# Performance work log

Measured on AMD Instinct MI355X. Metric: run time of the kernel, lower is better.

Reference implementation:

```python
import jax, jax.numpy as jnp
import numpy as np

N_NODES, N_GRAPHS, N_EDGES = 40960, 1024, 163840


def setup_inputs() -> dict:
    key = jax.random.key(0)
    ks = jax.random.split(key, 40)
    w = lambda k, s: jax.random.normal(k, s, jnp.float32) * 0.05
    inp = {
        "x": jax.random.normal(ks[0], (N_NODES, 78), jnp.float32),
        "edge_index": jax.random.randint(ks[1], (2, N_EDGES), 0, N_NODES, jnp.int32),
        "batch": jnp.repeat(jnp.arange(N_GRAPHS, dtype=jnp.int32), N_NODES // N_GRAPHS),
        "target1": jax.random.normal(ks[2], (N_GRAPHS, 750, 20), jnp.float32),
        "target2": jax.random.randint(ks[3], (N_GRAPHS, 750), 0, 26, jnp.int32),
        # GCN layers
        "W1": w(ks[4], (78, 78)), "b1": jnp.zeros((78,), jnp.float32),
        "W2": w(ks[5], (78, 156)), "b2": jnp.zeros((156,), jnp.float32),
        "W3": w(ks[6], (156, 312)), "b3": jnp.zeros((312,), jnp.float32),
        "Wg1": w(ks[7], (312, 1024)), "bg1": jnp.zeros((1024,), jnp.float32),
        "Wg2": w(ks[8], (1024, 128)), "bg2": jnp.zeros((128,), jnp.float32),
        # protein branch
        "emb": w(ks[9], (26, 128)),
        "Wc2": w(ks[10], (32, 750, 8)), "bc2": jnp.zeros((32,), jnp.float32),
        "Wxt2": w(ks[11], (32 * 121, 128)), "bxt2": jnp.zeros((128,), jnp.float32),
        "Wc1": w(ks[12], (32, 750, 8)), "bc1": jnp.zeros((32,), jnp.float32),
        "Wxt1": w(ks[13], (416, 128)), "bxt1": jnp.zeros((128,), jnp.float32),
        # fusion head
        "Wf1": w(ks[14], (384, 1024)), "bf1": jnp.zeros((1024,), jnp.float32),
        "Wf2": w(ks[15], (1024, 512)), "bf2": jnp.zeros((512,), jnp.float32),
        "Wo": w(ks[16], (512, 1)), "bo": jnp.zeros((1,), jnp.float32),
    }
    return inp


def _conv1d(x, w, b):
    # x: [B, C_in, L], w: [C_out, C_in, K] -> [B, C_out, L-K+1]
    y = jax.lax.conv_general_dilated(x, w, (1,), "VALID",
                                     dimension_numbers=("NCH", "OIH", "NCH"))
    return y + b[None, :, None]


def reference(x, edge_index, batch, target1, target2,
              W1, b1, W2, b2, W3, b3, Wg1, bg1, Wg2, bg2,
              emb, Wc2, bc2, Wxt2, bxt2, Wc1, bc1, Wxt1, bxt1,
              Wf1, bf1, Wf2, bf2, Wo, bo):
    N = x.shape[0]
    loop = jnp.arange(N, dtype=edge_index.dtype)
    src = jnp.concatenate([edge_index[0], loop])  # message source j
    dst = jnp.concatenate([edge_index[1], loop])  # aggregation target i
    # symmetric GCN normalization with self-loops (degree from dst, as in PyG)
    deg = jnp.zeros((N,), x.dtype).at[dst].add(1.0)
    dinv = jax.lax.rsqrt(deg)  # deg >= 1 due to self loops
    norm = (dinv[src] * dinv[dst])[:, None]

    def gcn(h, W, b):
        m = (h @ W)[src] * norm
        return jax.ops.segment_sum(m, dst, num_segments=N) + b

    h = jax.nn.relu(gcn(x, W1, b1))
    h = jax.nn.relu(gcn(h, W2, b2))
    h = jax.nn.relu(gcn(h, W3, b3))
    # global max pool per graph
    g = jax.ops.segment_max(h, batch, num_segments=N_GRAPHS)
    g = jax.nn.relu(g @ Wg1 + bg1)
    g = g @ Wg2 + bg2  # dropout is identity at inference

    # protein branch 2: embedding -> conv1d over channels=750
    e = emb[target2]                         # [B, 750, 128]
    xt2 = _conv1d(e, Wc2, bc2)               # [B, 32, 121]
    xt2 = xt2.reshape(-1, 32 * 121) @ Wxt2 + bxt2

    # protein branch 1: raw float features
    xt1 = _conv1d(target1, Wc1, bc1)         # [B, 32, 13]
    xt1 = xt1.reshape(-1, 416) @ Wxt1 + bxt1

    xc = jnp.concatenate([g, xt1, xt2], axis=1)  # [B, 384]
    xc = jax.nn.relu(xc @ Wf1 + bf1)
    xc = jax.nn.relu(xc @ Wf2 + bf2)
    return xc @ Wo + bo
```

## Files before the change

### kernel.cpp

```cpp
#include <hip/hip_runtime.h>
#include <hip/hip_bf16.h>

#define NN 40960
#define NE 163840
#define NB 1024

typedef __attribute__((ext_vector_type(8))) short short8;
typedef __attribute__((ext_vector_type(4))) short short4v;
typedef __attribute__((ext_vector_type(4))) float floatx4;

__device__ inline unsigned short f2bf(float f) {
    union { float f; unsigned u; } v; v.f = f;
    unsigned r = v.u + 0x7fffu + ((v.u >> 16) & 1u);
    return (unsigned short)(r >> 16);
}
__device__ inline float bf2f(unsigned short s) {
    union { unsigned u; float f; } v; v.u = ((unsigned)s) << 16; return v.f;
}
__device__ inline unsigned pack2bf(float lo, float hi) {
    return (unsigned)f2bf(lo) | ((unsigned)f2bf(hi) << 16);
}

static const size_t o_dinv = 0, o_g312 = 40960, o_g1024 = 360448, o_xc = 1409024,
                    o_f1 = 1802240, o_f2 = 2850816, o_b1v = 3375104, o_b2v = 3375232,
// ... 31 lines not shown
        int t = __shfl_up(s, d);
        if (l >= d) s += t;
    }
    if (l < 40) blockOff[l] = s - orig;
}

__global__ __launch_bounds__(1024) void k_scan3(int* __restrict__ off, int* __restrict__ cur,
                                                const int* __restrict__ blockOff) {
    int i = blockIdx.x * 1024 + threadIdx.x;
    int o = off[i] + blockOff[blockIdx.x];
    off[i] = o;
    cur[i] = o;
    if (i == NN - 1) off[NN] = NE;
}

__global__ void k_fill(const int* __restrict__ ei, int* __restrict__ cur, int* __restrict__ srcOut) {
    int e = blockIdx.x * 256 + threadIdx.x;
    if (e >= NE) return;
    int s = ei[e], d = ei[NE + e];
    int pos = atomicAdd(&cur[d], 1);
    srcOut[pos] = s;
}

__global__ __launch_bounds__(256) void k_cvt_wt(const float* __restrict__ W1, const float* __restrict__ W2,
                                                const float* __restrict__ W3, const float* __restrict__ Wg1,
                                                const float* __restrict__ Wg2, const float* __restrict__ Wf1,
                                                const float* __restrict__ Wf2, unsigned short* __restrict__ dst) {
    const int cum[8]  = {0, 128, 320, 640, 1664, 1792, 2816, 3328};
    const int KP[7]   = {96, 96, 160, 320, 1024, 384, 1024};
    const int KB[7]   = {78, 78, 156, 312, 1024, 384, 1024};
    const int NNm[7]  = {78, 156, 312, 1024, 128, 1024, 512};
    const size_t OFF[7] = {0, 12288, 30720, 81920, 409600, 540672, 933888};
    int m = 0;
    int bx = blockIdx.x;
    while (m < 6 && bx >= cum[m + 1]) m++;
    int r = bx - cum[m];
    const float* src = (m == 0) ? W1 : (m == 1) ? W2 : (m == 2) ? W3 : (m == 3) ? Wg1
                     : (m == 4) ? Wg2 : (m == 5) ? Wf1 : Wf2;
    int kp = KP[m], kb = KB[m], nn = NNm[m];
    unsigned short* d = dst + OFF[m] + (size_t)r * kp;
    for (int k = threadIdx.x; k < kp; k += 256) {
        float v = (r < nn && k < kb) ? src[(size_t)k * nn + r] : 0.f;
        d[k] = f2bf(v);
    }
}

__global__ __launch_bounds__(64) void k_agg_x(const float* __restrict__ x, const float* __restrict__ dinv,
                                              const int* __restrict__ off, const int* __restrict__ srcs,
                                              unsigned* __restrict__ out) {
    int n = blockIdx.x;
    int f = threadIdx.x;
    if (f >= 48) return;
    if (f >= 39) { out[(size_t)n * 48 + f] = 0; return; }
    float di = dinv[n];
    float2 sv = *(const float2*)&x[(size_t)n * 78 + 2 * f];
    float a0 = sv.x * di * di, a1 = sv.y * di * di;
    int e0 = off[n], e1 = off[n + 1];
    int e = e0;
    for (; e + 4 <= e1; e += 4) {
        int s0 = srcs[e], s1 = srcs[e + 1], s2 = srcs[e + 2], s3 = srcs[e + 3];
        float d0 = dinv[s0] * di, d1 = dinv[s1] * di, d2 = dinv[s2] * di, d3 = dinv[s3] * di;
        float2 v0 = *(const float2*)&x[(size_t)s0 * 78 + 2 * f];
        float2 v1 = *(const float2*)&x[(size_t)s1 * 78 + 2 * f];
        float2 v2 = *(const float2*)&x[(size_t)s2 * 78 + 2 * f];
        float2 v3 = *(const float2*)&x[(size_t)s3 * 78 + 2 * f];
        a0 += v0.x * d0 + v1.x * d1 + v2.x * d2 + v3.x * d3;
        a1 += v0.y * d0 + v1.y * d1 + v2.y * d2 + v3.y * d3;
    }
    for (; e < e1; e++) {
        int s = srcs[e];
        float dd = dinv[s] * di;
        float2 v = *(const float2*)&x[(size_t)s * 78 + 2 * f];
        a0 += v.x * dd; a1 += v.y * dd;
    }
    out[(size_t)n * 48 + f] = pack2bf(a0, a1);
}

__global__ void k_agg16(const unsigned* __restrict__ h, const float* __restrict__ dinv,
                        const int* __restrict__ off, const int* __restrict__ srcs,
                        unsigned* __restrict__ out, int F2) {
    int n = blockIdx.x;
    int f = threadIdx.x;
    if (f >= F2) return;
    float di = dinv[n];
    unsigned s0v = h[(size_t)n * F2 + f];
    float a0 = bf2f((unsigned short)(s0v & 0xffff)) * di * di;
    float a1 = bf2f((unsigned short)(s0v >> 16)) * di * di;
    int e0 = off[n], e1 = off[n + 1];
    int e = e0;
    for (; e + 4 <= e1; e += 4) {
        int s0 = srcs[e], s1 = srcs[e + 1], s2 = srcs[e + 2], s3 = srcs[e + 3];
        float d0 = dinv[s0] * di, d1 = dinv[s1] * di, d2 = dinv[s2] * di, d3 = dinv[s3] * di;
        unsigned v0 = h[(size_t)s0 * F2 + f];
        unsigned v1 = h[(size_t)s1 * F2 + f];
        unsigned v2 = h[(size_t)s2 * F2 + f];
        unsigned v3 = h[(size_t)s3 * F2 + f];
        a0 += bf2f((unsigned short)(v0 & 0xffff)) * d0 + bf2f((unsigned short)(v1 & 0xffff)) * d1
            + bf2f((unsigned short)(v2 & 0xffff)) * d2 + bf2f((unsigned short)(v3 & 0xffff)) * d3;
        a1 += bf2f((unsigned short)(v0 >> 16)) * d0 + bf2f((unsigned short)(v1 >> 16)) * d1
            + bf2f((unsigned short)(v2 >> 16)) * d2 + bf2f((unsigned short)(v3 >> 16)) * d3;
    }
    for (; e < e1; e++) {
        int s = srcs[e];
        float dd = dinv[s] * di;
        unsigned v = h[(size_t)s * F2 + f];
        a0 += bf2f((unsigned short)(v & 0xffff)) * dd;
        a1 += bf2f((unsigned short)(v >> 16)) * dd;
    }
    out[(size_t)n * F2 + f] = pack2bf(a0, a1);
}

__global__ void k_segmax16(const unsigned short* __restrict__ h, unsigned short* __restrict__ g) {
    int gr = blockIdx.x, f = threadIdx.x;
    if (f >= 320) return;
    if (f >= 312) { g[(size_t)gr * 320 + f] = 0; return; }
    float m = 0.0f;
    const unsigned short* base = h + (size_t)gr * 40 * 312 + f;
    for (int i = 0; i < 40; i++) m = fmaxf(m, bf2f(base[(size_t)i * 312]));
    g[(size_t)gr * 320 + f] = f2bf(m);
}

#define LDST 72
template <bool ABF16, bool OUTBF16, bool ATOMIC, bool RELU_OUT>
__global__ __launch_bounds__(256) void gemm_bt(const void* __restrict__ Av, const unsigned short* __restrict__ Bt,
                                               const float* __restrict__ bias, void* __restrict__ Cv,
                                               int Nn, int Npad, int Kpad, int Klim,
                                               int lda, int ldb, int ldc, int ksplit) {
    __shared__ __align__(16) unsigned short As[64 * LDST];
    __shared__ __align__(16) unsigned short Bs[64 * LDST];
    const float* Af = (const float*)Av;
    const unsigned short* A16 = (const unsigned short*)Av;
    float* Cf = (float*)Cv;
    unsigned short* C16 = (unsigned short*)Cv;
    int bn0 = blockIdx.x * 64;
    int bm0 = blockIdx.y * 64;
    int k0 = blockIdx.z * ksplit;
    int kend = k0 + ksplit; if (kend > Kpad) kend = Kpad;
    int tid = threadIdx.x;
    int w = tid >> 6, l = tid & 63, q = l >> 4, r = l & 15;
    int wr = w >> 1, wc = w & 1;

    floatx4 acc[2][2];
// ... 45 lines not shown
    for (int c2 = 0; c2 < 2; c2++) {
        int col = bn0 + wc * 32 + c2 * 16 + r;
        if (col >= Npad) continue;
        bool live = col < Nn;
        float bv = (bias && live) ? bias[col] : 0.f;
#pragma unroll
        for (int i = 0; i < 2; i++) {
#pragma unroll
            for (int v = 0; v < 4; v++) {
                int row = bm0 + wr * 32 + i * 16 + q * 4 + v;
                float val = live ? (acc[i][c2][v] + bv) : 0.f;
                if (RELU_OUT) val = fmaxf(val, 0.f);
                if (OUTBF16) {
                    C16[(size_t)row * ldc + col] = live ? f2bf(val) : (unsigned short)0;
                } else if (live) {
                    if (ATOMIC) atomicAdd(&Cf[(size_t)row * ldc + col], val);
                    else Cf[(size_t)row * ldc + col] = val;
                }
            }
        }
    }
}

#define T1LD 40
#define T1S  48
#define T1K  320
__global__ __launch_bounds__(256) void gemm_t1(const float* __restrict__ A, const unsigned short* __restrict__ Bt,
                                               float* __restrict__ P) {
    __shared__ __align__(16) unsigned short As[2][64 * T1LD];
    __shared__ __align__(16) unsigned short Bs[2][128 * T1LD];
    const int Klim = 15000;
    int bm0 = blockIdx.y * 64;
    int k0 = blockIdx.x * T1K;
    int tid = threadIdx.x;
    int w = tid >> 6, l = tid & 63, q = l >> 4, r = l & 15;
    int wr = w >> 1, wc = w & 1;

    floatx4 acc[2][4];
#pragma unroll
    for (int i = 0; i < 2; i++)
#pragma unroll
        for (int c = 0; c < 4; c++) acc[i][c] = (floatx4)0.0f;

    int ra = tid >> 3, ca = (tid & 7) * 4;
    int rb = tid >> 2, cb = (tid & 3) * 8;
    const float* Ap0 = A + (size_t)(bm0 + ra) * Klim + ca;
    const float* Ap1 = A + (size_t)(bm0 + ra + 32) * Klim + ca;
    const unsigned short* Bp0 = Bt + (size_t)rb * 15360 + cb;
    const unsigned short* Bp1 = Bt + (size_t)(rb + 64) * 15360 + cb;

    float4 aA0, aA1, aB0, aB1;
    short8 bA0, bA1, bB0, bB1;

    auto loadT = [&](int kt, float4& x0, float4& x1, short8& y0, short8& y1) {
        int c = kt + ca;
        if (c < Klim) {
            x0 = *(const float4*)(Ap0 + kt);
            x1 = *(const float4*)(Ap1 + kt);
        } else {
            x0 = make_float4(0.f, 0.f, 0.f, 0.f);
            x1 = make_float4(0.f, 0.f, 0.f, 0.f);
        }
        y0 = *(const short8*)(Bp0 + kt);
        y1 = *(const short8*)(Bp1 + kt);
    };
    auto stageW = [&](int buf, const float4& x0, const float4& x1, const short8& y0, const short8& y1) {
        short4v s0, s1;
        s0[0] = (short)f2bf(x0.x); s0[1] = (short)f2bf(x0.y); s0[2] = (short)f2bf(x0.z); s0[3] = (short)f2bf(x0.w);
        s1[0] = (short)f2bf(x1.x); s1[1] = (short)f2bf(x1.y); s1[2] = (short)f2bf(x1.z); s1[3] = (short)f2bf(x1.w);
        *(short4v*)&As[buf][ra * T1LD + ca] = s0;
        *(short4v*)&As[buf][(ra + 32) * T1LD + ca] = s1;
        *(short8*)&Bs[buf][rb * T1LD + cb] = y0;
        *(short8*)&Bs[buf][(rb + 64) * T1LD + cb] = y1;
    };
    auto compute = [&](int buf) {
        short8 a0 = *(const short8*)&As[buf][(wr * 32 + r) * T1LD + q * 8];
        short8 a1 = *(const short8*)&As[buf][(wr * 32 + 16 + r) * T1LD + q * 8];
        short8 b0 = *(const short8*)&Bs[buf][(wc * 64 + r) * T1LD + q * 8];
        short8 b1 = *(const short8*)&Bs[buf][(wc * 64 + 16 + r) * T1LD + q * 8];
        short8 b2 = *(const short8*)&Bs[buf][(wc * 64 + 32 + r) * T1LD + q * 8];
        short8 b3 = *(const short8*)&Bs[buf][(wc * 64 + 48 + r) * T1LD + q * 8];
        acc[0][0] = __builtin_amdgcn_mfma_f32_16x16x32_bf16(a0, b0, acc[0][0], 0, 0, 0);
        acc[0][1] = __builtin_amdgcn_mfma_f32_16x16x32_bf16(a0, b1, acc[0][1], 0, 0, 0);
        acc[0][2] = __builtin_amdgcn_mfma_f32_16x16x32_bf16(a0, b2, acc[0][2], 0, 0, 0);
        acc[0][3] = __builtin_amdgcn_mfma_f32_16x16x32_bf16(a0, b3, acc[0][3], 0, 0, 0);
        acc[1][0] = __builtin_amdgcn_mfma_f32_16x16x32_bf16(a1, b0, acc[1][0], 0, 0, 0);
        acc[1][1] = __builtin_amdgcn_mfma_f32_16x16x32_bf16(a1, b1, acc[1][1], 0, 0, 0);
        acc[1][2] = __builtin_amdgcn_mfma_f32_16x16x32_bf16(a1, b2, acc[1][2], 0, 0, 0);
        acc[1][3] = __builtin_amdgcn_mfma_f32_16x16x32_bf16(a1, b3, acc[1][3], 0, 0, 0);
    };

    loadT(k0, aA0, aA1, bA0, bA1);
    loadT(k0 + 32, aB0, aB1, bB0, bB1);
#pragma unroll
    for (int it = 0; it < T1K / 32; it += 2) {
        stageW(0, aA0, aA1, bA0, bA1);
        if (it + 2 < T1K / 32) loadT(k0 + (it + 2) * 32, aA0, aA1, bA0, bA1);
        asm volatile("s_waitcnt lgkmcnt(0)" ::: "memory");
        __builtin_amdgcn_s_barrier();
        asm volatile("" ::: "memory");
        compute(0);
        stageW(1, aB0, aB1, bB0, bB1);
        if (it + 3 < T1K / 32) loadT(k0 + (it + 3) * 32, aB0, aB1, bB0, bB1);
        asm volatile("s_waitcnt lgkmcnt(0)" ::: "memory");
        __builtin_amdgcn_s_barrier();
        asm volatile("" ::: "memory");
        compute(1);
    }

    float* Pp = P + (size_t)blockIdx.x * (1024 * 128) + (size_t)bm0 * 128;
#pragma unroll
    for (int c = 0; c < 4; c++) {
        int col = wc * 64 + c * 16 + r;
#pragma unroll
        for (int i = 0; i < 2; i++) {
#pragma unroll
            for (int v = 0; v < 4; v++) {
                int row = wr * 32 + i * 16 + q * 4 + v;
                Pp[(size_t)row * 128 + col] = acc[i][c][v];
            }
        }
    }
}

__global__ __launch_bounds__(128) void k_red_t1(const float* __restrict__ P, float* __restrict__ xc) {
    int row = blockIdx.x, j = threadIdx.x;
    const float* p = P + (size_t)row * 128 + j;
    float s = 0.f;
#pragma unroll
    for (int ks = 0; ks < T1S; ks++) s += p[(size_t)ks * (1024 * 128)];
    xc[(size_t)row * 384 + 128 + j] += s;
}

template <int OM>
__global__ __launch_bounds__(256) void gemm_mfma_batch(const float* __restrict__ A, const float* __restrict__ B,
                                                       void* __restrict__ Cv,
                                                       int M, int Nn, int K, int ldc,
                                                       long sB, long sC) {
    __shared__ __align__(16) unsigned short As[64 * LDST];
    __shared__ __align__(16) unsigned short Bs[64 * LDST];
    const float* Bm = B + (size_t)blockIdx.z * sB;
    unsigned short* C16 = (unsigned short*)Cv + (size_t)blockIdx.z * sC;
    int bn0 = blockIdx.x * 64;
    int bm0 = blockIdx.y * 64;
    int tid = threadIdx.x;
    int w = tid >> 6, l = tid & 63, q = l >> 4, r = l & 15;
    int wr = w >> 1, wc = w & 1;

    floatx4 acc[2][2];
#pragma unroll
    for (int i = 0; i < 2; i++)
#pragma unroll
        for (int c = 0; c < 2; c++) acc[i][c] = (floatx4)0.0f;

    int mA = tid >> 2, kcA = (tid & 3) * 8;
    int nB = tid >> 2, kcB = (tid & 3) * 8;
    int gmA = bm0 + mA;
    int gnB = bn0 + nB;

    for (int kt = 0; kt < K; kt += 32) {
        {
            float av[8];
            const float* Ap = A + (size_t)gmA * K + kt + kcA;
            if (gmA < M) {
#pragma unroll
// ... 22 lines not shown
        }
        __syncthreads();
        short8 a0 = *(const short8*)&As[(wr * 32 + r) * LDST + q * 8];
        short8 a1 = *(const short8*)&As[(wr * 32 + 16 + r) * LDST + q * 8];
        short8 b0 = *(const short8*)&Bs[(wc * 32 + r) * LDST + q * 8];
        short8 b1 = *(const short8*)&Bs[(wc * 32 + 16 + r) * LDST + q * 8];
        acc[0][0] = __builtin_amdgcn_mfma_f32_16x16x32_bf16(a0, b0, acc[0][0], 0, 0, 0);
        acc[0][1] = __builtin_amdgcn_mfma_f32_16x16x32_bf16(a0, b1, acc[0][1], 0, 0, 0);
        acc[1][0] = __builtin_amdgcn_mfma_f32_16x16x32_bf16(a1, b0, acc[1][0], 0, 0, 0);
        acc[1][1] = __builtin_amdgcn_mfma_f32_16x16x32_bf16(a1, b1, acc[1][1], 0, 0, 0);
        __syncthreads();
    }

#pragma unroll
    for (int c = 0; c < 2; c++) {
        int col = bn0 + wc * 32 + c * 16 + r;
        if (col >= Nn) continue;
#pragma unroll
        for (int i = 0; i < 2; i++) {
#pragma unroll
            for (int v = 0; v < 4; v++) {
                int row = bm0 + wr * 32 + i * 16 + q * 4 + v;
                if (row >= M) continue;
                if (OM == 1) C16[(size_t)row * ldc + col] = f2bf(acc[i][c][v]);
                else C16[(size_t)col * ldc + row * 20 + blockIdx.z] = f2bf(acc[i][c][v]);
            }
        }
    }
}

__global__ __launch_bounds__(256) void k_wcr_both(const float* __restrict__ Wc2, const float* __restrict__ Wc1,
                                                  float* __restrict__ Wc2r, float* __restrict__ Wc1r) {
    int cc = blockIdx.x, j = threadIdx.x;
    const float* W = (cc < 750) ? Wc2 : Wc1;
    float* Wr = (cc < 750) ? Wc2r : Wc1r;
    int c = (cc < 750) ? cc : cc - 750;
    Wr[(size_t)c * 256 + j] = W[(size_t)(j >> 3) * 6000 + c * 8 + (j & 7)];
}

__global__ __launch_bounds__(128) void k_T_build(const float* __restrict__ emb, const float* __restrict__ Wxt2,
                                                 float* __restrict__ T) {
    __shared__ float el[128];
    int v = blockIdx.x >> 5, o = blockIdx.x & 31, j = threadIdx.x;
    el[j] = emb[(size_t)v * 128 + j];
    __syncthreads();
    float acc[8] = {};
    for (int l = 0; l < 121; l++) {
        float w = Wxt2[(size_t)(o * 121 + l) * 128 + j];
#pragma unroll
        for (int k = 0; k < 8; k++) acc[k] += el[l + k] * w;
    }
#pragma unroll
    for (int k = 0; k < 8; k++) T[(size_t)(v * 256 + o * 8 + k) * 128 + j] = acc[k];
}

__global__ __launch_bounds__(128) void k_bt_build(const float* __restrict__ Wxt1, float* __restrict__ Bt) {
    int ok = blockIdx.x, t = blockIdx.y, j = threadIdx.x;
    int o = ok >> 3, k = ok & 7, lpos = t - k;
    float v = (lpos >= 0 && lpos < 13) ? Wxt1[(size_t)(o * 13 + lpos) * 128 + j] : 0.f;
    Bt[(size_t)(t * 256 + ok) * 128 + j] = v;
}

__global__ __launch_bounds__(128) void k_u_gather16(const int* __restrict__ t2, const unsigned short* __restrict__ U,
                                                    const float* __restrict__ b2v, float* __restrict__ xc) {
    __shared__ int offs[752];
    __shared__ float red[8][128];
    int b = blockIdx.x, tid = threadIdx.x;
    int rg = tid >> 4, lane = tid & 15;
    const int* t2b = t2 + (size_t)b * 750;
    for (int i = tid; i < 750; i += 128) offs[i] = i * 3328 + t2b[i] * 128;
    __syncthreads();
    float a[8] = {};
#pragma unroll 4
    for (int i = rg; i < 750; i += 8) {
        short8 v = *(const short8*)&U[(size_t)offs[i] + lane * 8];
#pragma unroll
        for (int c = 0; c < 8; c++) a[c] += bf2f((unsigned short)v[c]);
    }
#pragma unroll
    for (int c = 0; c < 8; c++) red[rg][lane * 8 + c] = a[c];
    __syncthreads();
    float s = b2v[tid];
#pragma unroll
    for (int g = 0; g < 8; g++) s += red[g][tid];
    xc[(size_t)b * 384 + 256 + tid] = s;
}

__global__ void k_bias_init(const float* __restrict__ bxt1, const float* __restrict__ bxt2,
                            float* __restrict__ b1v, float* __restrict__ b2v) {
    int j = threadIdx.x;
    b1v[j] = bxt1[j];
    b2v[j] = bxt2[j];
}

__global__ __launch_bounds__(128) void k_bias_acc_both(const float* __restrict__ bc1, const float* __restrict__ Wxt1,
                                                       float* __restrict__ b1v,
                                                       const float* __restrict__ bc2, const float* __restrict__ Wxt2,
                                                       float* __restrict__ b2v) {
    int b = blockIdx.x, j = threadIdx.x;
    if (b < 32) {
        const float* p = Wxt1 + (size_t)b * 13 * 128 + j;
        float t = 0.f;
        for (int l = 0; l < 13; l++) t += p[(size_t)l * 128];
        atomicAdd(&b1v[j], bc1[b] * t);
    } else {
        int o = b - 32;
        const float* p = Wxt2 + (size_t)o * 121 * 128 + j;
        float t = 0.f;
        for (int l = 0; l < 121; l++) t += p[(size_t)l * 128];
        atomicAdd(&b2v[j], bc2[o] * t);
    }
}

__global__ __launch_bounds__(768) void k_initC(float* __restrict__ xc, float* __restrict__ f2,
                                               const float* __restrict__ bg2, const float* __restrict__ b1v,
                                               const float* __restrict__ bf2) {
    int b = blockIdx.x, t = threadIdx.x;
    if (t < 128) xc[(size_t)b * 384 + t] = bg2[t];
    else if (t < 256) xc[(size_t)b * 384 + t] = b1v[t - 128];
    else f2[(size_t)b * 512 + t - 256] = bf2[t - 256];
}

__global__ __launch_bounds__(64) void k_final(const float* __restrict__ f2, const float* __restrict__ Wo,
                                              const float* __restrict__ bo, float* __restrict__ out) {
    int b = blockIdx.x, lane = threadIdx.x;
    float s = 0.f;
    for (int j = lane; j < 512; j += 64) s += fmaxf(f2[(size_t)b * 512 + j], 0.f) * Wo[j];
    for (int off = 32; off; off >>= 1) s += __shfl_down(s, off);
    if (lane == 0) out[b] = s + bo[0];
}

extern "C" void kernel_launch(void* const* d_in, const int* in_sizes, int n_in,
                              void* d_out, int out_size, void* d_ws, size_t ws_size,
// ... 32 lines not shown
    float* ws = (float*)d_ws;
    float* dinv  = ws + o_dinv;
    unsigned short* g312b = (unsigned short*)(ws + o_g312);
    unsigned short* g1024b = (unsigned short*)(ws + o_g1024);
    float* xc    = ws + o_xc;
    unsigned short* f1b = (unsigned short*)(ws + o_f1);
    float* f2    = ws + o_f2;
    float* b1v   = ws + o_b1v;
    float* b2v   = ws + o_b2v;
    int* csrOff  = (int*)(ws + o_iws);
    int* csrCur  = csrOff + (NN + 1);
    int* csrSrc  = csrCur + NN;
    int* blockSum = (int*)(ws + o_f1 + 600000);
    int* blockOff = blockSum + 40;
    float* bufA  = ws + o_bufA;
    float* bufB  = ws + o_bufB;
    float* T    = bufA;
    unsigned short* U16  = (unsigned short*)(bufA + 851968);
    unsigned short* Vt16 = (unsigned short*)(bufA + 2200000);
    unsigned short* Wt   = (unsigned short*)(bufA + 3200000);
    float* Wc2r = bufA + 4000000;
    float* Wc1r = bufA + 4200000;
    float* Btb  = bufA + 4400000;
    unsigned* aggb = (unsigned*)bufB;
    unsigned short* h16 = (unsigned short*)(bufB + 5500000);
    float* Pt1 = bufB;

    unsigned short* W1t  = Wt + 0;
    unsigned short* W2t  = Wt + 12288;
    unsigned short* W3t  = Wt + 30720;
    unsigned short* Wg1t = Wt + 81920;
    unsigned short* Wg2t = Wt + 409600;
    unsigned short* Wf1t = Wt + 540672;
    unsigned short* Wf2t = Wt + 933888;

    hipMemsetAsync(csrCur, 0, NN * sizeof(int), stream);
    k_hist<<<NE / 256, 256, 0, stream>>>(ei + NE, csrCur);
    k_scan1<<<40, 1024, 0, stream>>>(csrCur, csrOff, blockSum, dinv);
    k_scan2<<<1, 64, 0, stream>>>(blockSum, blockOff);
    k_scan3<<<40, 1024, 0, stream>>>(csrOff, csrCur, blockOff);
    k_fill<<<NE / 256, 256, 0, stream>>>(ei, csrCur, csrSrc);
    k_cvt_wt<<<3328, 256, 0, stream>>>(W1, W2, W3, Wg1, Wg2, Wf1, Wf2, Wt);

    k_agg_x<<<NN, 64, 0, stream>>>(x, dinv, csrOff, csrSrc, aggb);
    gemm_bt<true, true, false, true><<<dim3(2, 640, 1), 256, 0, stream>>>(
        aggb, W1t, b1, h16, 78, 96, 96, 96, 96, 96, 96, 96);
    k_agg16<<<NN, 64, 0, stream>>>((unsigned*)h16, dinv, csrOff, csrSrc, aggb, 48);
    gemm_bt<true, true, false, true><<<dim3(3, 640, 1), 256, 0, stream>>>(
        aggb, W2t, b2, h16, 156, 160, 96, 96, 96, 96, 160, 96);
    k_agg16<<<NN, 128, 0, stream>>>((unsigned*)h16, dinv, csrOff, csrSrc, aggb, 80);
    gemm_bt<true, true, false, true><<<dim3(5, 640, 1), 256, 0, stream>>>(
        aggb, W3t, b3, h16, 312, 312, 160, 160, 160, 160, 312, 160);
    k_segmax16<<<NB, 320, 0, stream>>>(h16, g312b);
    gemm_bt<true, true, false, true><<<dim3(16, 16, 1), 256, 0, stream>>>(
        g312b, Wg1t, bg1, g1024b, 1024, 1024, 320, 320, 320, 320, 1024, 320);

    k_bias_init<<<1, 128, 0, stream>>>(bxt1, bxt2, b1v, b2v);
    k_bias_acc_both<<<64, 128, 0, stream>>>(bc1, Wxt1, b1v, bc2, Wxt2, b2v);
    k_initC<<<NB, 768, 0, stream>>>(xc, f2, bg2, b1v, bf2);

    gemm_bt<true, false, true, false><<<dim3(2, 16, 8), 256, 0, stream>>>(
        g1024b, Wg2t, nullptr, xc + 0, 128, 128, 1024, 1024, 1024, 1024, 384, 128);

    k_wcr_both<<<1500, 256, 0, stream>>>(Wc2, Wc1, Wc2r, Wc1r);
    k_T_build<<<26 * 32, 128, 0, stream>>>(emb, Wxt2, T);
    gemm_mfma_batch<1><<<dim3(2, 12, 26), 256, 0, stream>>>(Wc2r, T, U16, 750, 128, 256, 3328, 32768, 128);
    k_u_gather16<<<NB, 128, 0, stream>>>(t2, U16, b2v, xc);

    k_bt_build<<<dim3(256, 20), 128, 0, stream>>>(Wxt1, Btb);
    hipMemsetAsync(Vt16, 0, (size_t)128 * 15360 * 2, stream);
    gemm_mfma_batch<2><<<dim3(2, 12, 20), 256, 0, stream>>>(Wc1r, Btb, Vt16, 750, 128, 256, 15360, 32768, 0);
    gemm_t1<<<dim3(T1S, 16, 1), 256, 0, stream>>>(t1, Vt16, Pt1);
    k_red_t1<<<NB, 128, 0, stream>>>(Pt1, xc);

    gemm_bt<false, true, false, true><<<dim3(16, 16, 1), 256, 0, stream>>>(
        xc, Wf1t, bf1, f1b, 1024, 1024, 384, 384, 384, 384, 1024, 384);
    gemm_bt<true, false, true, false><<<dim3(8, 16, 4), 256, 0, stream>>>(
        f1b, Wf2t, nullptr, f2, 512, 512, 1024, 1024, 1024, 1024, 512, 256);
    k_final<<<NB, 64, 0, stream>>>(f2, Wo, bo, out);
}
```

Before: 458.8 us.

## Merge independent kernels into combined launches to cut launch count and overlap branches

```diff
diff --git a/kernel.cpp b/kernel.cpp
--- a/kernel.cpp
+++ b/kernel.cpp
@@ -77,65 +77,91 @@
     srcOut[pos] = s;
 }
 
-__global__ __launch_bounds__(256) void k_cvt_wt(const float* __restrict__ W1, const float* __restrict__ W2,
-                                                const float* __restrict__ W3, const float* __restrict__ Wg1,
-                                                const float* __restrict__ Wg2, const float* __restrict__ Wf1,
-                                                const float* __restrict__ Wf2, unsigned short* __restrict__ dst) {
-    const int cum[8]  = {0, 128, 320, 640, 1664, 1792, 2816, 3328};
-    const int KP[7]   = {96, 96, 160, 320, 1024, 384, 1024};
-    const int KB[7]   = {78, 78, 156, 312, 1024, 384, 1024};
-    const int NNm[7]  = {78, 156, 312, 1024, 128, 1024, 512};
-    const size_t OFF[7] = {0, 12288, 30720, 81920, 409600, 540672, 933888};
-    int m = 0;
-    int bx = blockIdx.x;
-    while (m < 6 && bx >= cum[m + 1]) m++;
-    int r = bx - cum[m];
-    const float* src = (m == 0) ? W1 : (m == 1) ? W2 : (m == 2) ? W3 : (m == 3) ? Wg1
-                     : (m == 4) ? Wg2 : (m == 5) ? Wf1 : Wf2;
-    int kp = KP[m], kb = KB[m], nn = NNm[m];
-    unsigned short* d = dst + OFF[m] + (size_t)r * kp;
-    for (int k = threadIdx.x; k < kp; k += 256) {
-        float v = (r < nn && k < kb) ? src[(size_t)k * nn + r] : 0.f;
-        d[k] = f2bf(v);
-    }
-}
-
-__global__ __launch_bounds__(64) void k_agg_x(const float* __restrict__ x, const float* __restrict__ dinv,
-                                              const int* __restrict__ off, const int* __restrict__ srcs,
-                                              unsigned* __restrict__ out) {
-    int n = blockIdx.x;
-    int f = threadIdx.x;
-    if (f >= 48) return;
-    if (f >= 39) { out[(size_t)n * 48 + f] = 0; return; }
-    float di = dinv[n];
-    float2 sv = *(const float2*)&x[(size_t)n * 78 + 2 * f];
-    float a0 = sv.x * di * di, a1 = sv.y * di * di;
-    int e0 = off[n], e1 = off[n + 1];
-    int e = e0;
-    for (; e + 4 <= e1; e += 4) {
-        int s0 = srcs[e], s1 = srcs[e + 1], s2 = srcs[e + 2], s3 = srcs[e + 3];
-        float d0 = dinv[s0] * di, d1 = dinv[s1] * di, d2 = dinv[s2] * di, d3 = dinv[s3] * di;
-        float2 v0 = *(const float2*)&x[(size_t)s0 * 78 + 2 * f];
-        float2 v1 = *(const float2*)&x[(size_t)s1 * 78 + 2 * f];
-        float2 v2 = *(const float2*)&x[(size_t)s2 * 78 + 2 * f];
-        float2 v3 = *(const float2*)&x[(size_t)s3 * 78 + 2 * f];
-        a0 += v0.x * d0 + v1.x * d1 + v2.x * d2 + v3.x * d3;
-        a1 += v0.y * d0 + v1.y * d1 + v2.y * d2 + v3.y * d3;
-    }
-    for (; e < e1; e++) {
-        int s = srcs[e];
-        float dd = dinv[s] * di;
-        float2 v = *(const float2*)&x[(size_t)s * 78 + 2 * f];
-        a0 += v.x * dd; a1 += v.y * dd;
-    }
-    out[(size_t)n * 48 + f] = pack2bf(a0, a1);
-}
-
-__global__ void k_agg16(const unsigned* __restrict__ h, const float* __restrict__ dinv,
-                        const int* __restrict__ off, const int* __restrict__ srcs,
-                        unsigned* __restrict__ out, int F2) {
-    int n = blockIdx.x;
-    int f = threadIdx.x;
+__global__ __launch_bounds__(256) void k_prep_mega(
+    const float* __restrict__ W1, const float* __restrict__ W2, const float* __restrict__ W3,
+    const float* __restrict__ Wg1, const float* __restrict__ Wg2, const float* __restrict__ Wf1,
+    const float* __restrict__ Wf2, unsigned short* __restrict__ Wt,
+    const float* __restrict__ Wc2, const float* __restrict__ Wc1,
+    float* __restrict__ Wc2r, float* __restrict__ Wc1r,
+    const float* __restrict__ Wxt1, float* __restrict__ Btb,
+    const float* __restrict__ bc1, const float* __restrict__ bxt1, float* __restrict__ b1v,
+    const float* __restrict__ bc2, const float* __restrict__ Wxt2, const float* __restrict__ bxt2,
+    float* __restrict__ b2v,
+    const float* __restrict__ emb, float* __restrict__ T) {
+    __shared__ float el[128];
+    __shared__ float bsum[2][128];
+    int bx = blockIdx.x, tid = threadIdx.x;
+    if (bx < 3328) {
+        const int cum[8]  = {0, 128, 320, 640, 1664, 1792, 2816, 3328};
+        const int KP[7]   = {96, 96, 160, 320, 1024, 384, 1024};
+        const int KB[7]   = {78, 78, 156, 312, 1024, 384, 1024};
+        const int NNm[7]  = {78, 156, 312, 1024, 128, 1024, 512};
+        const size_t OFF[7] = {0, 12288, 30720, 81920, 409600, 540672, 933888};
+        int m = 0;
+        while (m < 6 && bx >= cum[m + 1]) m++;
+        int r = bx - cum[m];
+        const float* src = (m == 0) ? W1 : (m == 1) ? W2 : (m == 2) ? W3 : (m == 3) ? Wg1
+                         : (m == 4) ? Wg2 : (m == 5) ? Wf1 : Wf2;
+        int kp = KP[m], kb = KB[m], nn = NNm[m];
+        unsigned short* d = Wt + OFF[m] + (size_t)r * kp;
+        for (int k = tid; k < kp; k += 256) {
+            float v = (r < nn && k < kb) ? src[(size_t)k * nn + r] : 0.f;
+            d[k] = f2bf(v);
+        }
+    } else if (bx < 4828) {
+        int cc = bx - 3328, j = tid;
+        const float* W = (cc < 750) ? Wc2 : Wc1;
+        float* Wr = (cc < 750) ? Wc2r : Wc1r;
+        int c = (cc < 750) ? cc : cc - 750;
+        Wr[(size_t)c * 256 + j] = W[(size_t)(j >> 3) * 6000 + c * 8 + (j & 7)];
+    } else if (bx < 7388) {
+        int idx = (bx - 4828) * 256 + tid;
+        int j = idx & 127, ok = (idx >> 7) & 255, t = idx >> 15;
+        int o = ok >> 3, k = ok & 7, lpos = t - k;
+        float v = (lpos >= 0 && lpos < 13) ? Wxt1[(size_t)(o * 13 + lpos) * 128 + j] : 0.f;
+        Btb[(size_t)(t * 256 + ok) * 128 + j] = v;
+    } else if (bx == 7388) {
+        int o2 = tid >> 7, j = tid & 127;
+        float p = 0.f;
+        for (int o = o2; o < 32; o += 2) {
+            float t = 0.f;
+            for (int l = 0; l < 13; l++) t += Wxt1[(size_t)(o * 13 + l) * 128 + j];
+            p += bc1[o] * t;
+        }
+        bsum[o2][j] = p;
+        __syncthreads();
+        if (tid < 128) b1v[j] = bxt1[j] + bsum[0][j] + bsum[1][j];
+    } else if (bx == 7389) {
+        int o2 = tid >> 7, j = tid & 127;
+        float p = 0.f;
+        for (int o = o2; o < 32; o += 2) {
+            float t = 0.f;
+            for (int l = 0; l < 121; l++) t += Wxt2[(size_t)(o * 121 + l) * 128 + j];
+            p += bc2[o] * t;
+        }
+        bsum[o2][j] = p;
+        __syncthreads();
+        if (tid < 128) b2v[j] = bxt2[j] + bsum[0][j] + bsum[1][j];
+    } else {
+        int tb = bx - 7390;
+        int v = tb >> 4, op = tb & 15;
+        int o = op * 2 + (tid >> 7), j = tid & 127;
+        if (tid < 128) el[j] = emb[(size_t)v * 128 + j];
+        __syncthreads();
+        float acc[8] = {};
+        for (int l = 0; l < 121; l++) {
+            float w = Wxt2[(size_t)(o * 121 + l) * 128 + j];
+#pragma unroll
+            for (int k = 0; k < 8; k++) acc[k] += el[l + k] * w;
+        }
+#pragma unroll
+        for (int k = 0; k < 8; k++) T[(size_t)(v * 256 + o * 8 + k) * 128 + j] = acc[k];
+    }
+}
+
+__device__ inline void d_agg16_node(int n, int f, const unsigned* __restrict__ h,
+                                    const float* __restrict__ dinv, const int* __restrict__ off,
+                                    const int* __restrict__ srcs, unsigned* __restrict__ out, int F2) {
     if (f >= F2) return;
     float di = dinv[n];
     unsigned s0v = h[(size_t)n * F2 + f];
@@ -165,14 +191,10 @@
     out[(size_t)n * F2 + f] = pack2bf(a0, a1);
 }
 
-__global__ void k_segmax16(const unsigned short* __restrict__ h, unsigned short* __restrict__ g) {
-    int gr = blockIdx.x, f = threadIdx.x;
-    if (f >= 320) return;
-    if (f >= 312) { g[(size_t)gr * 320 + f] = 0; return; }
-    float m = 0.0f;
-    const unsigned short* base = h + (size_t)gr * 40 * 312 + f;
-    for (int i = 0; i < 40; i++) m = fmaxf(m, bf2f(base[(size_t)i * 312]));
-    g[(size_t)gr * 320 + f] = f2bf(m);
+__global__ void k_agg16(const unsigned* __restrict__ h, const float* __restrict__ dinv,
+                        const int* __restrict__ off, const int* __restrict__ srcs,
+                        unsigned* __restrict__ out, int F2) {
+    d_agg16_node(blockIdx.x, threadIdx.x, h, dinv, off, srcs, out, F2);
 }
 
 #define LDST 72
@@ -264,125 +286,19 @@
     }
 }
 
-#define T1LD 40
-#define T1S  48
-#define T1K  320
-__global__ __launch_bounds__(256) void gemm_t1(const float* __restrict__ A, const unsigned short* __restrict__ Bt,
-                                               float* __restrict__ P) {
-    __shared__ __align__(16) unsigned short As[2][64 * T1LD];
-    __shared__ __align__(16) unsigned short Bs[2][128 * T1LD];
-    const int Klim = 15000;
-    int bm0 = blockIdx.y * 64;
-    int k0 = blockIdx.x * T1K;
-    int tid = threadIdx.x;
-    int w = tid >> 6, l = tid & 63, q = l >> 4, r = l & 15;
-    int wr = w >> 1, wc = w & 1;
-
-    floatx4 acc[2][4];
-#pragma unroll
-    for (int i = 0; i < 2; i++)
-#pragma unroll
-        for (int c = 0; c < 4; c++) acc[i][c] = (floatx4)0.0f;
-
-    int ra = tid >> 3, ca = (tid & 7) * 4;
-    int rb = tid >> 2, cb = (tid & 3) * 8;
-    const float* Ap0 = A + (size_t)(bm0 + ra) * Klim + ca;
-    const float* Ap1 = A + (size_t)(bm0 + ra + 32) * Klim + ca;
-    const unsigned short* Bp0 = Bt + (size_t)rb * 15360 + cb;
-    const unsigned short* Bp1 = Bt + (size_t)(rb + 64) * 15360 + cb;
-
-    float4 aA0, aA1, aB0, aB1;
-    short8 bA0, bA1, bB0, bB1;
-
-    auto loadT = [&](int kt, float4& x0, float4& x1, short8& y0, short8& y1) {
-        int c = kt + ca;
-        if (c < Klim) {
-            x0 = *(const float4*)(Ap0 + kt);
-            x1 = *(const float4*)(Ap1 + kt);
-        } else {
-            x0 = make_float4(0.f, 0.f, 0.f, 0.f);
-            x1 = make_float4(0.f, 0.f, 0.f, 0.f);
-        }
-        y0 = *(const short8*)(Bp0 + kt);
-        y1 = *(const short8*)(Bp1 + kt);
-    };
-    auto stageW = [&](int buf, const float4& x0, const float4& x1, const short8& y0, const short8& y1) {
-        short4v s0, s1;
-        s0[0] = (short)f2bf(x0.x); s0[1] = (short)f2bf(x0.y); s0[2] = (short)f2bf(x0.z); s0[3] = (short)f2bf(x0.w);
-        s1[0] = (short)f2bf(x1.x); s1[1] = (short)f2bf(x1.y); s1[2] = (short)f2bf(x1.z); s1[3] = (short)f2bf(x1.w);
-        *(short4v*)&As[buf][ra * T1LD + ca] = s0;
-        *(short4v*)&As[buf][(ra + 32) * T1LD + ca] = s1;
-        *(short8*)&Bs[buf][rb * T1LD + cb] = y0;
-        *(short8*)&Bs[buf][(rb + 64) * T1LD + cb] = y1;
-    };
-    auto compute = [&](int buf) {
-        short8 a0 = *(const short8*)&As[buf][(wr * 32 + r) * T1LD + q * 8];
-        short8 a1 = *(const short8*)&As[buf][(wr * 32 + 16 + r) * T1LD + q * 8];
-        short8 b0 = *(const short8*)&Bs[buf][(wc * 64 + r) * T1LD + q * 8];
-        short8 b1 = *(const short8*)&Bs[buf][(wc * 64 + 16 + r) * T1LD + q * 8];
-        short8 b2 = *(const short8*)&Bs[buf][(wc * 64 + 32 + r) * T1LD + q * 8];
-        short8 b3 = *(const short8*)&Bs[buf][(wc * 64 + 48 + r) * T1LD + q * 8];
-        acc[0][0] = __builtin_amdgcn_mfma_f32_16x16x32_bf16(a0, b0, acc[0][0], 0, 0, 0);
-        acc[0][1] = __builtin_amdgcn_mfma_f32_16x16x32_bf16(a0, b1, acc[0][1], 0, 0, 0);
-        acc[0][2] = __builtin_amdgcn_mfma_f32_16x16x32_bf16(a0, b2, acc[0][2], 0, 0, 0);
-        acc[0][3] = __builtin_amdgcn_mfma_f32_16x16x32_bf16(a0, b3, acc[0][3], 0, 0, 0);
-        acc[1][0] = __builtin_amdgcn_mfma_f32_16x16x32_bf16(a1, b0, acc[1][0], 0, 0, 0);
-        acc[1][1] = __builtin_amdgcn_mfma_f32_16x16x32_bf16(a1, b1, acc[1][1], 0, 0, 0);
-        acc[1][2] = __builtin_amdgcn_mfma_f32_16x16x32_bf16(a1, b2, acc[1][2], 0, 0, 0);
-        acc[1][3] = __builtin_amdgcn_mfma_f32_16x16x32_bf16(a1, b3, acc[1][3], 0, 0, 0);
-    };
-
-    loadT(k0, aA0, aA1, bA0, bA1);
-    loadT(k0 + 32, aB0, aB1, bB0, bB1);
-#pragma unroll
-    for (int it = 0; it < T1K / 32; it += 2) {
-        stageW(0, aA0, aA1, bA0, bA1);
-        if (it + 2 < T1K / 32) loadT(k0 + (it + 2) * 32, aA0, aA1, bA0, bA1);
-        asm volatile("s_waitcnt lgkmcnt(0)" ::: "memory");
-        __builtin_amdgcn_s_barrier();
-        asm volatile("" ::: "memory");
-        compute(0);
-        stageW(1, aB0, aB1, bB0, bB1);
-        if (it + 3 < T1K / 32) loadT(k0 + (it + 3) * 32, aB0, aB1, bB0, bB1);
-        asm volatile("s_waitcnt lgkmcnt(0)" ::: "memory");
-        __builtin_amdgcn_s_barrier();
-        asm volatile("" ::: "memory");
-        compute(1);
-    }
-
-    float* Pp = P + (size_t)blockIdx.x * (1024 * 128) + (size_t)bm0 * 128;
-#pragma unroll
-    for (int c = 0; c < 4; c++) {
-        int col = wc * 64 + c * 16 + r;
-#pragma unroll
-        for (int i = 0; i < 2; i++) {
-#pragma unroll
-            for (int v = 0; v < 4; v++) {
-                int row = wr * 32 + i * 16 + q * 4 + v;
-                Pp[(size_t)row * 128 + col] = acc[i][c][v];
-            }
-        }
-    }
-}
-
-__global__ __launch_bounds__(128) void k_red_t1(const float* __restrict__ P, float* __restrict__ xc) {
-    int row = blockIdx.x, j = threadIdx.x;
-    const float* p = P + (size_t)row * 128 + j;
-    float s = 0.f;
-#pragma unroll
-    for (int ks = 0; ks < T1S; ks++) s += p[(size_t)ks * (1024 * 128)];
-    xc[(size_t)row * 384 + 128 + j] += s;
-}
-
-template <int OM>
-__global__ __launch_bounds__(256) void gemm_mfma_batch(const float* __restrict__ A, const float* __restrict__ B,
-                                                       void* __restrict__ Cv,
-                                                       int M, int Nn, int K, int ldc,
-                                                       long sB, long sC) {
+__global__ __launch_bounds__(256) void k_batch_both(const float* __restrict__ Wc2r, const float* __restrict__ T,
+                                                    const float* __restrict__ Wc1r, const float* __restrict__ Btb,
+                                                    unsigned short* __restrict__ U16, unsigned short* __restrict__ Vt16) {
     __shared__ __align__(16) unsigned short As[64 * LDST];
     __shared__ __align__(16) unsigned short Bs[64 * LDST];
-    const float* Bm = B + (size_t)blockIdx.z * sB;
-    unsigned short* C16 = (unsigned short*)Cv + (size_t)blockIdx.z * sC;
+    const int M = 750, Nn = 128, K = 256;
+    int z = blockIdx.z;
+    bool om1 = z < 26;
+    const float* A = om1 ? Wc2r : Wc1r;
+    const float* Bm = om1 ? (T + (size_t)z * 32768) : (Btb + (size_t)(z - 26) * 32768);
+    unsigned short* C16 = om1 ? (U16 + (size_t)z * 128) : Vt16;
+    int ldc = om1 ? 3328 : 15360;
+    int zz = z - 26;
     int bn0 = blockIdx.x * 64;
     int bm0 = blockIdx.y * 64;
     int tid = threadIdx.x;
@@ -451,93 +367,199 @@
             for (int v = 0; v < 4; v++) {
                 int row = bm0 + wr * 32 + i * 16 + q * 4 + v;
                 if (row >= M) continue;
-                if (OM == 1) C16[(size_t)row * ldc + col] = f2bf(acc[i][c][v]);
-                else C16[(size_t)col * ldc + row * 20 + blockIdx.z] = f2bf(acc[i][c][v]);
+                if (om1) C16[(size_t)row * ldc + col] = f2bf(acc[i][c][v]);
+                else C16[(size_t)col * ldc + row * 20 + zz] = f2bf(acc[i][c][v]);
             }
         }
     }
 }
 
-__global__ __launch_bounds__(256) void k_wcr_both(const float* __restrict__ Wc2, const float* __restrict__ Wc1,
-                                                  float* __restrict__ Wc2r, float* __restrict__ Wc1r) {
-    int cc = blockIdx.x, j = threadIdx.x;
-    const float* W = (cc < 750) ? Wc2 : Wc1;
-    float* Wr = (cc < 750) ? Wc2r : Wc1r;
-    int c = (cc < 750) ? cc : cc - 750;
-    Wr[(size_t)c * 256 + j] = W[(size_t)(j >> 3) * 6000 + c * 8 + (j & 7)];
-}
-
-__global__ __launch_bounds__(128) void k_T_build(const float* __restrict__ emb, const float* __restrict__ Wxt2,
-                                                 float* __restrict__ T) {
-    __shared__ float el[128];
-    int v = blockIdx.x >> 5, o = blockIdx.x & 31, j = threadIdx.x;
-    el[j] = emb[(size_t)v * 128 + j];
-    __syncthreads();
-    float acc[8] = {};
-    for (int l = 0; l < 121; l++) {
-        float w = Wxt2[(size_t)(o * 121 + l) * 128 + j];
-#pragma unroll
-        for (int k = 0; k < 8; k++) acc[k] += el[l + k] * w;
-    }
-#pragma unroll
-    for (int k = 0; k < 8; k++) T[(size_t)(v * 256 + o * 8 + k) * 128 + j] = acc[k];
-}
-
-__global__ __launch_bounds__(128) void k_bt_build(const float* __restrict__ Wxt1, float* __restrict__ Bt) {
-    int ok = blockIdx.x, t = blockIdx.y, j = threadIdx.x;
-    int o = ok >> 3, k = ok & 7, lpos = t - k;
-    float v = (lpos >= 0 && lpos < 13) ? Wxt1[(size_t)(o * 13 + lpos) * 128 + j] : 0.f;
-    Bt[(size_t)(t * 256 + ok) * 128 + j] = v;
-}
-
-__global__ __launch_bounds__(128) void k_u_gather16(const int* __restrict__ t2, const unsigned short* __restrict__ U,
-                                                    const float* __restrict__ b2v, float* __restrict__ xc) {
+#define T1LD 40
+#define T1S  48
+#define T1K  320
+__global__ __launch_bounds__(256) void k_aggx_t1(
+    const float* __restrict__ x, const float* __restrict__ dinv, const int* __restrict__ off,
+    const int* __restrict__ srcs, unsigned* __restrict__ aggb,
+    const float* __restrict__ t1A, const unsigned short* __restrict__ Bt, float* __restrict__ P) {
+    __shared__ __align__(16) unsigned short As[2][64 * T1LD];
+    __shared__ __align__(16) unsigned short Bs[2][128 * T1LD];
+    int bx = blockIdx.x, tid = threadIdx.x;
+    if (bx < 768) {
+        const int Klim = 15000;
+        int mt = bx & 15, ks = bx >> 4;
+        int bm0 = mt * 64;
+        int k0 = ks * T1K;
+        int w = tid >> 6, l = tid & 63, q = l >> 4, r = l & 15;
+        int wr = w >> 1, wc = w & 1;
+
+        floatx4 acc[2][4];
+#pragma unroll
+        for (int i = 0; i < 2; i++)
+#pragma unroll
+            for (int c = 0; c < 4; c++) acc[i][c] = (floatx4)0.0f;
+
+        int ra = tid >> 3, ca = (tid & 7) * 4;
+        int rb = tid >> 2, cb = (tid & 3) * 8;
+        const float* Ap0 = t1A + (size_t)(bm0 + ra) * Klim + ca;
+        const float* Ap1 = t1A + (size_t)(bm0 + ra + 32) * Klim + ca;
+        const unsigned short* Bp0 = Bt + (size_t)rb * 15360 + cb;
+        const unsigned short* Bp1 = Bt + (size_t)(rb + 64) * 15360 + cb;
+
+        float4 aA0, aA1, aB0, aB1;
+        short8 bA0, bA1, bB0, bB1;
+
+        auto loadT = [&](int kt, float4& x0, float4& x1, short8& y0, short8& y1) {
+            int c = kt + ca;
+            if (c < Klim) {
+                x0 = *(const float4*)(Ap0 + kt);
+                x1 = *(const float4*)(Ap1 + kt);
+            } else {
+                x0 = make_float4(0.f, 0.f, 0.f, 0.f);
+                x1 = make_float4(0.f, 0.f, 0.f, 0.f);
+            }
+            y0 = *(const short8*)(Bp0 + kt);
+            y1 = *(const short8*)(Bp1 + kt);
+        };
+        auto stageW = [&](int buf, const float4& x0, const float4& x1, const short8& y0, const short8& y1) {
+            short4v s0, s1;
+            s0[0] = (short)f2bf(x0.x); s0[1] = (short)f2bf(x0.y); s0[2] = (short)f2bf(x0.z); s0[3] = (short)f2bf(x0.w);
+            s1[0] = (short)f2bf(x1.x); s1[1] = (short)f2bf(x1.y); s1[2] = (short)f2bf(x1.z); s1[3] = (short)f2bf(x1.w);
+            *(short4v*)&As[buf][ra * T1LD + ca] = s0;
+            *(short4v*)&As[buf][(ra + 32) * T1LD + ca] = s1;
+            *(short8*)&Bs[buf][rb * T1LD + cb] = y0;
+            *(short8*)&Bs[buf][(rb + 64) * T1LD + cb] = y1;
+        };
+        auto compute = [&](int buf) {
+            short8 a0 = *(const short8*)&As[buf][(wr * 32 + r) * T1LD + q * 8];
+            short8 a1 = *(const short8*)&As[buf][(wr * 32 + 16 + r) * T1LD + q * 8];
+            short8 b0 = *(const short8*)&Bs[buf][(wc * 64 + r) * T1LD + q * 8];
+            short8 b1 = *(const short8*)&Bs[buf][(wc * 64 + 16 + r) * T1LD + q * 8];
+            short8 b2 = *(const short8*)&Bs[buf][(wc * 64 + 32 + r) * T1LD + q * 8];
+            short8 b3 = *(const short8*)&Bs[buf][(wc * 64 + 48 + r) * T1LD + q * 8];
+            acc[0][0] = __builtin_amdgcn_mfma_f32_16x16x32_bf16(a0, b0, acc[0][0], 0, 0, 0);
+            acc[0][1] = __builtin_amdgcn_mfma_f32_16x16x32_bf16(a0, b1, acc[0][1], 0, 0, 0);
+            acc[0][2] = __builtin_amdgcn_mfma_f32_16x16x32_bf16(a0, b2, acc[0][2], 0, 0, 0);
+            acc[0][3] = __builtin_amdgcn_mfma_f32_16x16x32_bf16(a0, b3, acc[0][3], 0, 0, 0);
+            acc[1][0] = __builtin_amdgcn_mfma_f32_16x16x32_bf16(a1, b0, acc[1][0], 0, 0, 0);
+            acc[1][1] = __builtin_amdgcn_mfma_f32_16x16x32_bf16(a1, b1, acc[1][1], 0, 0, 0);
+            acc[1][2] = __builtin_amdgcn_mfma_f32_16x16x32_bf16(a1, b2, acc[1][2], 0, 0, 0);
+            acc[1][3] = __builtin_amdgcn_mfma_f32_16x16x32_bf16(a1, b3, acc[1][3], 0, 0, 0);
+        };
+
+        loadT(k0, aA0, aA1, bA0, bA1);
+        loadT(k0 + 32, aB0, aB1, bB0, bB1);
+#pragma unroll
+        for (int it = 0; it < T1K / 32; it += 2) {
+            stageW(0, aA0, aA1, bA0, bA1);
+            if (it + 2 < T1K / 32) loadT(k0 + (it + 2) * 32, aA0, aA1, bA0, bA1);
+            asm volatile("s_waitcnt lgkmcnt(0)" ::: "memory");
+            __builtin_amdgcn_s_barrier();
+            asm volatile("" ::: "memory");
+            compute(0);
+            stageW(1, aB0, aB1, bB0, bB1);
+            if (it + 3 < T1K / 32) loadT(k0 + (it + 3) * 32, aB0, aB1, bB0, bB1);
+            asm volatile("s_waitcnt lgkmcnt(0)" ::: "memory");
+            __builtin_amdgcn_s_barrier();
+            asm volatile("" ::: "memory");
+            compute(1);
+        }
+
+        float* Pp = P + (size_t)ks * (1024 * 128) + (size_t)bm0 * 128;
+#pragma unroll
+        for (int c = 0; c < 4; c++) {
+            int col = wc * 64 + c * 16 + r;
+#pragma unroll
+            for (int i = 0; i < 2; i++) {
+#pragma unroll
+                for (int v = 0; v < 4; v++) {
+                    int row = wr * 32 + i * 16 + q * 4 + v;
+                    Pp[(size_t)row * 128 + col] = acc[i][c][v];
+                }
+            }
+        }
+    } else {
+        int n = (bx - 768) * 4 + (tid >> 6);
+        int f = tid & 63;
+        if (f >= 48) return;
+        if (f >= 39) { aggb[(size_t)n * 48 + f] = 0; return; }
+        float di = dinv[n];
+        float2 sv = *(const float2*)&x[(size_t)n * 78 + 2 * f];
+        float a0 = sv.x * di * di, a1 = sv.y * di * di;
+        int e0 = off[n], e1 = off[n + 1];
+        int e = e0;
+        for (; e + 4 <= e1; e += 4) {
+            int s0 = srcs[e], s1 = srcs[e + 1], s2 = srcs[e + 2], s3 = srcs[e + 3];
+            float d0 = dinv[s0] * di, d1 = dinv[s1] * di, d2 = dinv[s2] * di, d3 = dinv[s3] * di;
+            float2 v0 = *(const float2*)&x[(size_t)s0 * 78 + 2 * f];
+            float2 v1 = *(const float2*)&x[(size_t)s1 * 78 + 2 * f];
+            float2 v2 = *(const float2*)&x[(size_t)s2 * 78 + 2 * f];
+            float2 v3 = *(const float2*)&x[(size_t)s3 * 78 + 2 * f];
+            a0 += v0.x * d0 + v1.x * d1 + v2.x * d2 + v3.x * d3;
+            a1 += v0.y * d0 + v1.y * d1 + v2.y * d2 + v3.y * d3;
+        }
+        for (; e < e1; e++) {
+            int s = srcs[e];
+            float dd = dinv[s] * di;
+            float2 v = *(const float2*)&x[(size_t)s * 78 + 2 * f];
+            a0 += v.x * dd; a1 += v.y * dd;
+        }
+        aggb[(size_t)n * 48 + f] = pack2bf(a0, a1);
+    }
+}
+
+__global__ __launch_bounds__(128) void k_agg16_ug(
+    const unsigned* __restrict__ h, const float* __restrict__ dinv, const int* __restrict__ off,
+    const int* __restrict__ srcs, unsigned* __restrict__ outb,
+    const int* __restrict__ t2, const unsigned short* __restrict__ U,
+    const float* __restrict__ b2v, float* __restrict__ xc) {
     __shared__ int offs[752];
     __shared__ float red[8][128];
-    int b = blockIdx.x, tid = threadIdx.x;
-    int rg = tid >> 4, lane = tid & 15;
-    const int* t2b = t2 + (size_t)b * 750;
-    for (int i = tid; i < 750; i += 128) offs[i] = i * 3328 + t2b[i] * 128;
-    __syncthreads();
-    float a[8] = {};
+    int bx = blockIdx.x, tid = threadIdx.x;
+    if (bx < NB) {
+        int b = bx;
+        int rg = tid >> 4, lane = tid & 15;
+        const int* t2b = t2 + (size_t)b * 750;
+        for (int i = tid; i < 750; i += 128) offs[i] = i * 3328 + t2b[i] * 128;
+        __syncthreads();
+        float a[8] = {};
 #pragma unroll 4
-    for (int i = rg; i < 750; i += 8) {
-        short8 v = *(const short8*)&U[(size_t)offs[i] + lane * 8];
-#pragma unroll
-        for (int c = 0; c < 8; c++) a[c] += bf2f((unsigned short)v[c]);
-    }
-#pragma unroll
-    for (int c = 0; c < 8; c++) red[rg][lane * 8 + c] = a[c];
-    __syncthreads();
-    float s = b2v[tid];
-#pragma unroll
-    for (int g = 0; g < 8; g++) s += red[g][tid];
-    xc[(size_t)b * 384 + 256 + tid] = s;
-}
-
-__global__ void k_bias_init(const float* __restrict__ bxt1, const float* __restrict__ bxt2,
-                            float* __restrict__ b1v, float* __restrict__ b2v) {
-    int j = threadIdx.x;
-    b1v[j] = bxt1[j];
-    b2v[j] = bxt2[j];
-}
-
-__global__ __launch_bounds__(128) void k_bias_acc_both(const float* __restrict__ bc1, const float* __restrict__ Wxt1,
-                                                       float* __restrict__ b1v,
-                                                       const float* __restrict__ bc2, const float* __restrict__ Wxt2,
-                                                       float* __restrict__ b2v) {
-    int b = blockIdx.x, j = threadIdx.x;
-    if (b < 32) {
-        const float* p = Wxt1 + (size_t)b * 13 * 128 + j;
-        float t = 0.f;
-        for (int l = 0; l < 13; l++) t += p[(size_t)l * 128];
-        atomicAdd(&b1v[j], bc1[b] * t);
+        for (int i = rg; i < 750; i += 8) {
+            short8 v = *(const short8*)&U[(size_t)offs[i] + lane * 8];
+#pragma unroll
+            for (int c = 0; c < 8; c++) a[c] += bf2f((unsigned short)v[c]);
+        }
+#pragma unroll
+        for (int c = 0; c < 8; c++) red[rg][lane * 8 + c] = a[c];
+        __syncthreads();
+        float s = b2v[tid];
+#pragma unroll
+        for (int g = 0; g < 8; g++) s += red[g][tid];
+        xc[(size_t)b * 384 + 256 + tid] = s;
     } else {
-        int o = b - 32;
-        const float* p = Wxt2 + (size_t)o * 121 * 128 + j;
-        float t = 0.f;
-        for (int l = 0; l < 121; l++) t += p[(size_t)l * 128];
-        atomicAdd(&b2v[j], bc2[o] * t);
+        d_agg16_node(bx - NB, tid, h, dinv, off, srcs, outb, 80);
+    }
+}
+
+__global__ void k_segmax_red(const unsigned short* __restrict__ h, unsigned short* __restrict__ g,
+                             const float* __restrict__ P, float* __restrict__ xc) {
+    int bx = blockIdx.x, tid = threadIdx.x;
+    if (bx < NB) {
+        if (tid < 128) {
+            int row = bx, j = tid;
+            const float* p = P + (size_t)row * 128 + j;
+            float s = 0.f;
+#pragma unroll
+            for (int ks = 0; ks < T1S; ks++) s += p[(size_t)ks * (1024 * 128)];
+            xc[(size_t)row * 384 + 128 + j] += s;
+        }
+    } else {
+        int gr = bx - NB, f = tid;
+        if (f >= 320) return;
+        if (f >= 312) { g[(size_t)gr * 320 + f] = 0; return; }
+        float m = 0.0f;
+        const unsigned short* base = h + (size_t)gr * 40 * 312 + f;
+        for (int i = 0; i < 40; i++) m = fmaxf(m, bf2f(base[(size_t)i * 312]));
+        g[(size_t)gr * 320 + f] = f2bf(m);
     }
 }
 
@@ -616,9 +638,9 @@
     float* Wc2r = bufA + 4000000;
     float* Wc1r = bufA + 4200000;
     float* Btb  = bufA + 4400000;
+    float* Pt1  = bufA + 6000000;
     unsigned* aggb = (unsigned*)bufB;
     unsigned short* h16 = (unsigned short*)(bufB + 5500000);
-    float* Pt1 = bufB;
 
     unsigned short* W1t  = Wt + 0;
     unsigned short* W2t  = Wt + 12288;
@@ -628,44 +650,40 @@
     unsigned short* Wf1t = Wt + 540672;
     unsigned short* Wf2t = Wt + 933888;
 
+    hipMemsetAsync(Vt16, 0, (size_t)128 * 15360 * 2, stream);
     hipMemsetAsync(csrCur, 0, NN * sizeof(int), stream);
     k_hist<<<NE / 256, 256, 0, stream>>>(ei + NE, csrCur);
     k_scan1<<<40, 1024, 0, stream>>>(csrCur, csrOff, blockSum, dinv);
     k_scan2<<<1, 64, 0, stream>>>(blockSum, blockOff);
     k_scan3<<<40, 1024, 0, stream>>>(csrOff, csrCur, blockOff);
     k_fill<<<NE / 256, 256, 0, stream>>>(ei, csrCur, csrSrc);
-    k_cvt_wt<<<3328, 256, 0, stream>>>(W1, W2, W3, Wg1, Wg2, Wf1, Wf2, Wt);
-
-    k_agg_x<<<NN, 64, 0, stream>>>(x, dinv, csrOff, csrSrc, aggb);
+
+    k_prep_mega<<<7806, 256, 0, stream>>>(W1, W2, W3, Wg1, Wg2, Wf1, Wf2, Wt,
+                                          Wc2, Wc1, Wc2r, Wc1r,
+                                          Wxt1, Btb, bc1, bxt1, b1v,
+                                          bc2, Wxt2, bxt2, b2v, emb, T);
+
+    k_batch_both<<<dim3(2, 12, 46), 256, 0, stream>>>(Wc2r, T, Wc1r, Btb, U16, Vt16);
+
+    k_initC<<<NB, 768, 0, stream>>>(xc, f2, bg2, b1v, bf2);
+
+    k_aggx_t1<<<768 + NN / 4, 256, 0, stream>>>(x, dinv, csrOff, csrSrc, aggb, t1, Vt16, Pt1);
+
     gemm_bt<true, true, false, true><<<dim3(2, 640, 1), 256, 0, stream>>>(
         aggb, W1t, b1, h16, 78, 96, 96, 96, 96, 96, 96, 96);
     k_agg16<<<NN, 64, 0, stream>>>((unsigned*)h16, dinv, csrOff, csrSrc, aggb, 48);
     gemm_bt<true, true, false, true><<<dim3(3, 640, 1), 256, 0, stream>>>(
         aggb, W2t, b2, h16, 156, 160, 96, 96, 96, 96, 160, 96);
-    k_agg16<<<NN, 128, 0, stream>>>((unsigned*)h16, dinv, csrOff, csrSrc, aggb, 80);
+    k_agg16_ug<<<NB + NN, 128, 0, stream>>>((unsigned*)h16, dinv, csrOff, csrSrc, aggb,
+                                            t2, U16, b2v, xc);
     gemm_bt<true, true, false, true><<<dim3(5, 640, 1), 256, 0, stream>>>(
         aggb, W3t, b3, h16, 312, 312, 160, 160, 160, 160, 312, 160);
-    k_segmax16<<<NB, 320, 0, stream>>>(h16, g312b);
+    k_segmax_red<<<2 * NB, 320, 0, stream>>>(h16, g312b, Pt1, xc);
     gemm_bt<true, true, false, true><<<dim3(16, 16, 1), 256, 0, stream>>>(
         g312b, Wg1t, bg1, g1024b, 1024, 1024, 320, 320, 320, 320, 1024, 320);
 
-    k_bias_init<<<1, 128, 0, stream>>>(bxt1, bxt2, b1v, b2v);
-    k_bias_acc_both<<<64, 128, 0, stream>>>(bc1, Wxt1, b1v, bc2, Wxt2, b2v);
-    k_initC<<<NB, 768, 0, stream>>>(xc, f2, bg2, b1v, bf2);
-
     gemm_bt<true, false, true, false><<<dim3(2, 16, 8), 256, 0, stream>>>(
         g1024b, Wg2t, nullptr, xc + 0, 128, 128, 1024, 1024, 1024, 1024, 384, 128);
-
-    k_wcr_both<<<1500, 256, 0, stream>>>(Wc2, Wc1, Wc2r, Wc1r);
-    k_T_build<<<26 * 32, 128, 0, stream>>>(emb, Wxt2, T);
-    gemm_mfma_batch<1><<<dim3(2, 12, 26), 256, 0, stream>>>(Wc2r, T, U16, 750, 128, 256, 3328, 32768, 128);
-    k_u_gather16<<<NB, 128, 0, stream>>>(t2, U16, b2v, xc);
-
-    k_bt_build<<<dim3(256, 20), 128, 0, stream>>>(Wxt1, Btb);
-    hipMemsetAsync(Vt16, 0, (size_t)128 * 15360 * 2, stream);
-    gemm_mfma_batch<2><<<dim3(2, 12, 20), 256, 0, stream>>>(Wc1r, Btb, Vt16, 750, 128, 256, 15360, 32768, 0);
-    gemm_t1<<<dim3(T1S, 16, 1), 256, 0, stream>>>(t1, Vt16, Pt1);
-    k_red_t1<<<NB, 128, 0, stream>>>(Pt1, xc);
 
     gemm_bt<false, true, false, true><<<dim3(16, 16, 1), 256, 0, stream>>>(
         xc, Wf1t, bf1, f1b, 1024, 1024, 384, 384, 384, 384, 1024, 384);
```

Result: slower. 489.4 us (+6.7%).
